# Kernel optimization log

Hardware: AMD Instinct MI355X
Metric: run time of the kernel (lower is better)

The kernel has to match this reference:

```python
import jax, jax.numpy as jnp
import numpy as np

Nq, Ns, D, H, S, B, MS, MB = 30000, 400, 128, 128, 200, 256, 4, 4
P = H + 3 * D  # pred_in_feature = 512


def _lin(k, out_f, in_f):
    sc = 1.0 / np.sqrt(in_f)
    return sc * jax.random.normal(k, (out_f, in_f), jnp.float32)


def setup_inputs() -> dict:
    key = jax.random.key(0)
    ks = jax.random.split(key, 40)
    inp = {}
    inp['q_emb'] = 0.1 * jax.random.normal(ks[0], (Nq, D), jnp.float32)
    inp['s_emb'] = 0.1 * jax.random.normal(ks[1], (Ns, D), jnp.float32)
    inp['ans_emb'] = jax.random.normal(ks[2], (4, D), jnp.float32)
    inp['label_emb'] = jax.random.normal(ks[3], (2, D), jnp.float32)
    inp['gru_Wi'] = _lin(ks[4], 3 * H, 5 * D)
    inp['gru_Wh'] = _lin(ks[5], 3 * H, H)
    inp['gru_bi'] = jnp.zeros((3 * H,), jnp.float32)
    inp['gru_bh'] = jnp.zeros((3 * H,), jnp.float32)
    for i, nm in enumerate(['s2s', 's2q', 'q2q', 'q2s']):
        inp[nm + '_W'] = _lin(ks[6 + i], D, D)
        inp[nm + '_b'] = jnp.zeros((D,), jnp.float32)
    inp['l1_W'] = _lin(ks[10], P, P); inp['l1_b'] = jnp.zeros((P,), jnp.float32)
    inp['l2_W'] = _lin(ks[11], P, P); inp['l2_b'] = jnp.zeros((P,), jnp.float32)
    inp['out_W'] = _lin(ks[12], 1, P); inp['out_b'] = jnp.zeros((1,), jnp.float32)
    inp['test_mask'] = jnp.ones((S, B), jnp.float32)
    inp['valid_mask'] = jnp.ones((S, B), jnp.float32)
    inp['local_test_mask'] = jnp.ones((S, B), jnp.float32)
    inp['subject_mask'] = jnp.ones((S, B, MB), jnp.float32)
    inp['q_mask'] = jnp.ones((Nq, MS), jnp.float32)
    inp['labels'] = jnp.round(jax.random.uniform(ks[13], (S, B), jnp.float32))
    inp['ans'] = jax.random.randint(ks[14], (S, B), 0, 4, jnp.int32)
    inp['correct_ans'] = jax.random.randint(ks[15], (S, B), 0, 4, jnp.int32)
    inp['subject_ids'] = jax.random.randint(ks[16], (S, B, MB), 0, Ns, jnp.int32)
    inp['q_ids'] = jax.random.randint(ks[17], (S, B), 0, Nq, jnp.int32)
    q_map = jax.random.randint(ks[18], (Nq, MS), 0, Ns, jnp.int32)
    inp['q_map'] = q_map
    inp['edge_q'] = jnp.repeat(jnp.arange(Nq, dtype=jnp.int32), MS)  # [Nq*MS]
    inp['edge_s'] = q_map.reshape(-1)  # subject segment id per edge
    return inp


def reference(q_emb, s_emb, ans_emb, label_emb, gru_Wi, gru_Wh, gru_bi, gru_bh,
              s2s_W, s2s_b, s2q_W, s2q_b, q2q_W, q2q_b, q2s_W, q2s_b,
              l1_W, l1_b, l2_W, l2_b, out_W, out_b,
              test_mask, valid_mask, local_test_mask, subject_mask, q_mask, labels,
              ans, correct_ans, subject_ids, q_ids, q_map, edge_q, edge_s):
    n_subject = s_emb.shape[0]
    # --- GCN layer 1: question -> subject aggregation (fused segment mean) ---
    q2s_proj = q_emb @ q2s_W.T + q2s_b                      # [Nq, D]
    sums = jax.ops.segment_sum(q2s_proj[edge_q], edge_s, num_segments=n_subject)
    cnts = jax.ops.segment_sum(jnp.ones_like(edge_s, q_emb.dtype), edge_s,
                               num_segments=n_subject)       # [Ns]
    nq_s = sums / jnp.maximum(cnts, 1.0)[:, None]            # mean over neighbor questions
    sq_s = s_emb @ s2s_W.T + s2s_b
    subjects_1 = jnp.where(cnts[:, None] > 0, jnp.tanh(nq_s + sq_s), 0.0)  # [Ns, D]
    # --- GCN layer 2: subject -> question aggregation ---
    nq = jnp.sum(subjects_1[q_map] * q_mask[..., None], axis=1) / \
         jnp.sum(q_mask, axis=-1, keepdims=True)             # [Nq, D]
    questions_1 = jnp.tanh(nq @ s2q_W.T + s2q_b + q_emb @ q2q_W.T + q2q_b)
    # --- sequence features ---
    mask = (test_mask * valid_mask * local_test_mask)[..., None]  # [S,B,1]
    subjects = jnp.sum(subjects_1[subject_ids] * subject_mask[..., None], axis=2)  # [S,B,D]
    questions = questions_1[q_ids]                            # [S,B,D]
    ans_embed = ans_emb[ans] * mask
    correct_ans_embed = ans_emb[correct_ans]
    label_embed = label_emb[labels.astype(jnp.int32)] * mask
    lstm_input = jnp.concatenate(
        [ans_embed, correct_ans_embed, label_embed, questions, subjects], axis=-1)  # [S,B,5D]
    # --- GRU (PyTorch gate layout: r|z|n), dropout=0 / eval mode ---
    xp = lstm_input @ gru_Wi.T + gru_bi                      # [S,B,3H]
    hdim = gru_Wh.shape[1]
    h0 = jnp.zeros((lstm_input.shape[1], hdim), lstm_input.dtype)

    def step(h, xp_t):
        gh = h @ gru_Wh.T + gru_bh
        xr, xz, xn = jnp.split(xp_t, 3, axis=-1)
        hr, hz, hn = jnp.split(gh, 3, axis=-1)
        r = jax.nn.sigmoid(xr + hr)
        z = jax.nn.sigmoid(xz + hz)
        n = jnp.tanh(xn + r * hn)
        h_new = (1.0 - z) * n + z * h
        return h_new, h_new

    _, outs = jax.lax.scan(step, h0, xp)                     # [S,B,H]
    forward_ht = jnp.concatenate([h0[None], outs[:-1]], axis=0)  # shifted hidden states
    # --- prediction head with residual ---
    pred_input = jnp.concatenate(
        [questions, subjects, forward_ht, correct_ans_embed], axis=-1)  # [S,B,P]
    h1 = jax.nn.relu(pred_input @ l1_W.T + l1_b)
    h2 = jax.nn.relu(h1 @ l2_W.T + l2_b)
    logits = ((h2 + pred_input) @ out_W.T + out_b)[..., 0]   # [S,B]
    # BCEWithLogits: softplus(x) - x*y
    per_elem = jax.nn.softplus(logits) - logits * labels
    mask2d = mask[..., 0]
    loss = jnp.mean(per_elem * mask2d) / jnp.mean(mask2d)
    probs = jax.nn.sigmoid(logits)
    return loss, probs
```

## Files before the change

kernel.cpp:

```cpp
#include <hip/hip_runtime.h>
#include <hip/hip_bf16.h>
#include <math.h>

#define NQ 30000
#define NS 400
#define DD 128
#define HH 128
#define SS 200
#define BB 256
#define MSq 4
#define MBs 4
#define PP 512
#define SB (SS*BB)
#define G3 384
#define QPB 16
#define REPL 8
#define TST (48*2048)

typedef __hip_bfloat16 bf16;
typedef __attribute__((ext_vector_type(8))) short bf16x8;
typedef __attribute__((ext_vector_type(4))) float f32x4;
typedef __attribute__((ext_vector_type(4))) _Float16 f16x4;

__device__ __forceinline__ float sigf(float x){ return 1.0f/(1.0f+expf(-x)); }
__device__ __forceinline__ float sigf2(float x){ return 1.0f/(1.0f+__expf(-x)); }
__device__ __forceinline__ float tanhf2(float x){ return 1.0f - 2.0f/(__expf(2.0f*x)+1.0f); }

__global__ __launch_bounds__(128) void tables_k(const float* __restrict__ ans_emb,
        const float* __restrict__ label_emb, const float* __restrict__ Wi,
        float* __restrict__ Tans, float* __restrict__ Tcae, float* __restrict__ Tlab){
  int j = blockIdx.x*128 + threadIdx.x;
  if (j >= G3) return;
  const float* wr = Wi + (size_t)j*640;
  for (int a=0;a<4;a++){
    float acc=0.f;
    for (int k=0;k<DD;k++) acc += ans_emb[a*DD+k]*wr[k];
    Tans[a*G3+j]=acc;
  }
  for (int a=0;a<4;a++){
    float acc=0.f;
    for (int k=0;k<DD;k++) acc += ans_emb[a*DD+k]*wr[128+k];
    Tcae[a*G3+j]=acc;
  }
  for (int l=0;l<2;l++){
    float acc=0.f;
    for (int k=0;k<DD;k++) acc += label_emb[l*DD+k]*wr[256+k];
    Tlab[l*G3+j]=acc;
  }
}

__global__ __launch_bounds__(256) void conv_w_k(const float* __restrict__ l1W,
        const float* __restrict__ l2W, const float* __restrict__ Wi,
        bf16* __restrict__ l1Wb, bf16* __restrict__ l2Wb, bf16* __restrict__ WiB){
  int i = blockIdx.x*256 + threadIdx.x;
  if (i < 512*512){
    l1Wb[i] = __float2bfloat16(l1W[i]);
    l2Wb[i] = __float2bfloat16(l2W[i]);
  }
  if (i < 384*256){
    int j = i >> 8, k = i & 255;
    WiB[i] = __float2bfloat16(Wi[j*640 + 384 + k]);
  }
}

__global__ __launch_bounds__(128) void q2s_scatter(const float* __restrict__ q_emb,
        const float* __restrict__ W, const float* __restrict__ bias,
        const int* __restrict__ q_map, float* __restrict__ sums, float* __restrict__ cnts){
  __shared__ float qe[QPB][DD];
  int q0 = blockIdx.x*QPB;
  int tid = threadIdx.x;
  float* S = sums + (size_t)(blockIdx.x & (REPL-1))*51200;
  float* C = cnts + (size_t)(blockIdx.x & (REPL-1))*400;
  for (int r=0;r<QPB;r++) qe[r][tid] = q_emb[(size_t)(q0+r)*DD + tid];
  __syncthreads();
  float acc[QPB];
  #pragma unroll
  for (int r=0;r<QPB;r++) acc[r] = bias[tid];
  const float4* wr = (const float4*)(W + (size_t)tid*DD);
  #pragma unroll 4
  for (int k4=0;k4<DD/4;k4++){
    float4 w = wr[k4];
    #pragma unroll
    for (int r=0;r<QPB;r++){
      acc[r] += w.x*qe[r][k4*4] + w.y*qe[r][k4*4+1] + w.z*qe[r][k4*4+2] + w.w*qe[r][k4*4+3];
    }
  }
  for (int r=0;r<QPB;r++){
    int q = q0+r;
    #pragma unroll
    for (int m=0;m<MSq;m++){
      int s = q_map[q*MSq+m];
      atomicAdd(&S[(size_t)s*DD + tid], acc[r]);
      if (tid==0) atomicAdd(&C[s], 1.0f);
    }
  }
}

__global__ __launch_bounds__(128) void subjects1_k(const float* __restrict__ s_emb,
        const float* __restrict__ W, const float* __restrict__ bias,
        const float* __restrict__ sums, const float* __restrict__ cnts,
        float* __restrict__ out){
  __shared__ float se[DD];
  int s = blockIdx.x; int tid = threadIdx.x;
  se[tid] = s_emb[(size_t)s*DD+tid];
  __syncthreads();
  float acc = bias[tid];
  const float4* wr = (const float4*)(W + (size_t)tid*DD);
  for (int k4=0;k4<DD/4;k4++){
    float4 w = wr[k4];
    acc += w.x*se[k4*4] + w.y*se[k4*4+1] + w.z*se[k4*4+2] + w.w*se[k4*4+3];
  }
  float c = 0.f, sm = 0.f;
  #pragma unroll
  for (int r=0;r<REPL;r++){
    c  += cnts[r*400 + s];
    sm += sums[(size_t)r*51200 + (size_t)s*DD + tid];
  }
  float v = 0.f;
  if (c > 0.f) v = tanhf(sm/fmaxf(c,1.f) + acc);
  out[(size_t)s*DD+tid] = v;
}

__global__ __launch_bounds__(128) void questions1_k(const float* __restrict__ q_emb,
        const float* __restrict__ subj1, const int* __restrict__ q_map,
        const float* __restrict__ q_mask,
        const float* __restrict__ s2qW, const float* __restrict__ s2qb,
        const float* __restrict__ q2qW, const float* __restrict__ q2qb,
        bf16* __restrict__ q1out){
  __shared__ float qe[QPB][DD];
  __shared__ float nq[QPB][DD];
  int q0 = blockIdx.x*QPB; int tid = threadIdx.x;
  for (int r=0;r<QPB;r++){
    int q = q0+r;
    qe[r][tid] = q_emb[(size_t)q*DD+tid];
    float sum=0.f, wsum=0.f;
    #pragma unroll
    for (int m=0;m<MSq;m++){
      float w = q_mask[q*MSq+m];
      sum += subj1[(size_t)q_map[q*MSq+m]*DD + tid]*w;
      wsum += w;
    }
    nq[r][tid] = sum / wsum;
  }
  __syncthreads();
  float acc[QPB];
  #pragma unroll
  for (int r=0;r<QPB;r++) acc[r] = s2qb[tid]+q2qb[tid];
  const float4* w1 = (const float4*)(s2qW + (size_t)tid*DD);
  const float4* w2 = (const float4*)(q2qW + (size_t)tid*DD);
  #pragma unroll 2
  for (int k4=0;k4<DD/4;k4++){
    float4 a = w1[k4]; float4 b = w2[k4];
    #pragma unroll
    for (int r=0;r<QPB;r++){
      acc[r] += a.x*nq[r][k4*4] + a.y*nq[r][k4*4+1] + a.z*nq[r][k4*4+2] + a.w*nq[r][k4*4+3]
              + b.x*qe[r][k4*4] + b.y*qe[r][k4*4+1] + b.z*qe[r][k4*4+2] + b.w*qe[r][k4*4+3];
    }
  }
  for (int r=0;r<QPB;r++) q1out[(size_t)(q0+r)*DD+tid] = __float2bfloat16(tanhf(acc[r]));
}

__global__ __launch_bounds__(128) void assemble_k(const bf16* __restrict__ q1,
        const float* __restrict__ subj1, const float* __restrict__ ans_emb,
        const int* __restrict__ cans, const int* __restrict__ sub_ids,
        const float* __restrict__ sub_mask, const int* __restrict__ q_ids,
        bf16* __restrict__ pred){
  int i = blockIdx.x; int d = threadIdx.x;
  size_t base = (size_t)i*PP;
  pred[base + d] = q1[(size_t)q_ids[i]*DD + d];
  float s = 0.f;
  #pragma unroll
  for (int m=0;m<MBs;m++)
    s += subj1[(size_t)sub_ids[i*MBs+m]*DD+d]*sub_mask[i*MBs+m];
  pred[base+128+d] = __float2bfloat16(s);
  pred[base+384+d] = __float2bfloat16(ans_emb[(size_t)cans[i]*DD + d]);
}

#define MFMA_CORE(A_, lda_, B_, ldb_, K_) \
  int lane = threadIdx.x & 63; int wid = threadIdx.x >> 6; \
  int wy = wid >> 1, wx = wid & 1; \
  int mbase = blockIdx.x*128 + wy*64; \
  int nbase = blockIdx.y*128 + wx*64; \
  int lr = lane & 15, kg = (lane >> 4) * 8; \
  f32x4 acc[4][4]; \
  _Pragma("unroll") for (int i=0;i<4;i++) _Pragma("unroll") for (int j=0;j<4;j++) acc[i][j] = (f32x4){0.f,0.f,0.f,0.f}; \
  for (int k=0; k<(K_); k+=32){ \
    bf16x8 af[4], bfr[4]; \
    _Pragma("unroll") for (int mi=0;mi<4;mi++) \
      af[mi] = *(const bf16x8*)((A_) + (size_t)(mbase+mi*16+lr)*(lda_) + k + kg); \
    _Pragma("unroll") for (int ni=0;ni<4;ni++) \
      bfr[ni] = *(const bf16x8*)((B_) + (size_t)(nbase+ni*16+lr)*(ldb_) + k + kg); \
    _Pragma("unroll") for (int mi=0;mi<4;mi++) \
      _Pragma("unroll") for (int ni=0;ni<4;ni++) \
        acc[mi][ni] = __builtin_amdgcn_mfma_f32_16x16x32_bf16(af[mi], bfr[ni], acc[mi][ni], 0, 0, 0); \
  }

__global__ __launch_bounds__(256) void gemm_xp(const bf16* __restrict__ pred,
        const bf16* __restrict__ WiB, const float* __restrict__ bi,
        const float* __restrict__ bh,
        const float* __restrict__ Tans, const float* __restrict__ Tcae,
        const float* __restrict__ Tlab,
        const float* __restrict__ tm, const float* __restrict__ vm,
        const float* __restrict__ lm,
        const int* __restrict__ ans, const int* __restrict__ cans,
        const float* __restrict__ labels, _Float16* __restrict__ xp2){
  MFMA_CORE(pred, PP, WiB, 256, 256)
  #pragma unroll
  for (int mi=0;mi<4;mi++){
    #pragma unroll
    for (int r=0;r<4;r++){
      int row = mbase + mi*16 + (lane>>4)*4 + r;
      int t = row >> 8, b = row & 255;
      size_t rowpart = ((size_t)t*48 + (b>>4)*3)*2048 + (b&15);
      float mk = tm[row]*vm[row]*lm[row];
      int a = ans[row], ca = cans[row], lb = (int)labels[row];
      #pragma unroll
      for (int ni=0;ni<4;ni++){
        int c = nbase + ni*16 + lr;
        int g = c >> 7, dd = c & 127;
        float v = acc[mi][ni][r] + bi[c]
            + mk*Tans[a*G3+c] + Tcae[ca*G3+c] + mk*Tlab[lb*G3+c];
        if (g < 2) v += bh[c];
        xp2[rowpart + (size_t)(g*2048 + dd*16)] = (_Float16)v;
      }
    }
  }
}

__global__ __launch_bounds__(256) void gemm_l1(const bf16* __restrict__ pred,
        const bf16* __restrict__ Wb, const float* __restrict__ bias,
        bf16* __restrict__ h1){
  MFMA_CORE(pred, PP, Wb, PP, PP)
  #pragma unroll
  for (int mi=0;mi<4;mi++){
    #pragma unroll
    for (int ni=0;ni<4;ni++){
      int c = nbase + ni*16 + lr;
      float bia = bias[c];
      #pragma unroll
      for (int r=0;r<4;r++){
        int row = mbase + mi*16 + (lane>>4)*4 + r;
        h1[(size_t)row*PP + c] = __float2bfloat16(fmaxf(acc[mi][ni][r] + bia, 0.f));
      }
    }
  }
}

__global__ __launch_bounds__(256) void gemm_l2_logits(const bf16* __restrict__ h1,
        const bf16* __restrict__ Wb, const float* __restrict__ bias,
        const bf16* __restrict__ pred, const float* __restrict__ outW,
        float* __restrict__ logits){
  MFMA_CORE(h1, PP, Wb, PP, PP)
  #pragma unroll
  for (int mi=0;mi<4;mi++){
    #pragma unroll
    for (int r=0;r<4;r++){
      int row = mbase + mi*16 + (lane>>4)*4 + r;
      float p = 0.f;
      #pragma unroll
      for (int ni=0;ni<4;ni++){
        int c = nbase + ni*16 + lr;
        float h2v = fmaxf(acc[mi][ni][r] + bias[c], 0.f);
        p += (h2v + __bfloat162float(pred[(size_t)row*PP + c])) * outW[c];
      }
      p += __shfl_xor(p,1);
      p += __shfl_xor(p,2);
      p += __shfl_xor(p,4);
      p += __shfl_xor(p,8);
      if (lr == 0) atomicAdd(&logits[row], p);
    }
  }
}

__global__ __launch_bounds__(512, 1) void gru_scan_mfma(const _Float16* __restrict__ xp2,
        const float* __restrict__ Wh, const float* __restrict__ bh,
        bf16* __restrict__ pred){
  __shared__ __align__(16) char hbf[8192];
  const int tid  = threadIdx.x;
  const int lane = tid & 63;
  const int w    = tid >> 6;
  const int lr   = lane & 15;
  const int lg   = lane >> 4;
  const int d    = w*16 + lr;
  const int bg0  = blockIdx.x * 16;

  union U8 { bf16x8 v; unsigned short s[8]; };
  bf16x8 wf0[4], wf1[4], wf2[4];
  #pragma unroll
  for (int kk=0; kk<4; kk++){
    #pragma unroll
    for (int g=0; g<3; g++){
      const float* src = Wh + (size_t)(g*HH + d)*HH + kk*32 + lg*8;
      U8 u;
      #pragma unroll
      for (int j=0;j<8;j++){
        bf16 bv = __float2bfloat16(src[j]);
        u.s[j] = reinterpret_cast<unsigned short&>(bv);
      }
      if (g==0) wf0[kk]=u.v; else if (g==1) wf1[kk]=u.v; else wf2[kk]=u.v;
    }
  }
  const float bh2 = bh[2*HH+d];

  int rdaddr[4];
  #pragma unroll
  for (int kk=0;kk<4;kk++) rdaddr[kk] = lr*256 + ((kk*64 + lg*16) ^ ((lr&7)<<4));
  int wraddr[4];
  #pragma unroll
  for (int q=0;q<4;q++){
    int B_ = lg*4 + q;
    wraddr[q] = B_*256 + ((2*d) ^ ((B_&7)<<4));
  }
  const int fB = tid >> 4, fblk = tid & 15;
  const int faddr = fB*256 + ((fblk*16) ^ ((fB&7)<<4));
  bf16* fptr = pred + ((size_t)bg0 + fB)*PP + 256 + fblk*8;
  const size_t PSTRIDE = (size_t)BB*PP;

  float h0=0.f, h1v=0.f, h2v=0.f, h3v=0.f;
  ((unsigned long long*)hbf)[tid]       = 0ULL;
  ((unsigned long long*)hbf)[tid + 512] = 0ULL;

  const _Float16* x0 = xp2 + (size_t)blockIdx.x*3*2048 + d*16 + lg*4;
  f16x4 xrA = *(const f16x4*)(x0);
  f16x4 xzA = *(const f16x4*)(x0 + 2048);
  f16x4 xnA = *(const f16x4*)(x0 + 4096);
  f16x4 xrB = *(const f16x4*)(x0 + TST);
  f16x4 xzB = *(const f16x4*)(x0 + TST + 2048);
  f16x4 xnB = *(const f16x4*)(x0 + TST + 4096);
  const _Float16* xtr = x0 + 2*(size_t)TST;
  const _Float16* xtz = xtr + 2048;
  const _Float16* xtn = xtr + 4096;

  __syncthreads();

#define GATEQ(Q, CR, CZ, CN, HV) { \
    float r  = sigf2((float)(CR) + ac0[Q]); \
    float zg = sigf2((float)(CZ) + ac1[Q]); \
    float n  = tanhf2((float)(CN) + r*(ac2[Q] + bh2)); \
    HV = (1.f - zg)*n + zg*HV; }

#define GSTEP(RO_, WO_, XR, XZ, XN) { \
    f32x4 ac0 = (f32x4){0.f,0.f,0.f,0.f}, ac1 = ac0, ac2 = ac0; \
    _Pragma("unroll") for (int kk=0; kk<4; kk++){ \
      bf16x8 a = *(const bf16x8*)(hbf + (RO_) + rdaddr[kk]); \
      ac0 = __builtin_amdgcn_mfma_f32_16x16x32_bf16(a, wf0[kk], ac0, 0,0,0); \
      ac1 = __builtin_amdgcn_mfma_f32_16x16x32_bf16(a, wf1[kk], ac1, 0,0,0); \
      ac2 = __builtin_amdgcn_mfma_f32_16x16x32_bf16(a, wf2[kk], ac2, 0,0,0); \
    } \
    if (tid < 256){   \
      int4 hv = *(const int4*)(hbf + (RO_) + faddr); \
      *(int4*)fptr = hv; \
    } \
    fptr += PSTRIDE; \
    GATEQ(0, (XR).x, (XZ).x, (XN).x, h0) \
    GATEQ(1, (XR).y, (XZ).y, (XN).y, h1v) \
    GATEQ(2, (XR).z, (XZ).z, (XN).z, h2v) \
    GATEQ(3, (XR).w, (XZ).w, (XN).w, h3v) \
    *(bf16*)(hbf + (WO_) + wraddr[0]) = __float2bfloat16(h0); \
    *(bf16*)(hbf + (WO_) + wraddr[1]) = __float2bfloat16(h1v); \
    *(bf16*)(hbf + (WO_) + wraddr[2]) = __float2bfloat16(h2v); \
    *(bf16*)(hbf + (WO_) + wraddr[3]) = __float2bfloat16(h3v); \
    XR = *(const f16x4*)(xtr); XZ = *(const f16x4*)(xtz); XN = *(const f16x4*)(xtn); \
    xtr += TST; xtz += TST; xtn += TST; \
    asm volatile("s_waitcnt lgkmcnt(0)" ::: "memory"); \
    __builtin_amdgcn_s_barrier(); \
    __builtin_amdgcn_sched_barrier(0); \
  }

  for (int t=0; t<SS; t+=2){
    GSTEP(0,    4096, xrA, xzA, xnA)
    GSTEP(4096, 0,    xrB, xzB, xnB)
  }
#undef GSTEP
#undef GATEQ
}

__global__ __launch_bounds__(256) void loss_probs_k(const float* __restrict__ logits,
        const float* __restrict__ labels, const float* __restrict__ tm,
        const float* __restrict__ vm, const float* __restrict__ lm,
        const float* __restrict__ out_b, float* __restrict__ out,
        float* __restrict__ lacc){
  int i = blockIdx.x*256 + threadIdx.x;
  float x = logits[i] + out_b[0];
  float lb = labels[i];
  float mk = tm[i]*vm[i]*lm[i];
  float sp = fmaxf(x,0.f) + log1pf(expf(-fabsf(x)));
  float pe = (sp - x*lb)*mk;
  out[1+i] = sigf(x);
  float v0 = pe, v1 = mk;
  for (int o=32;o>0;o>>=1){ v0 += __shfl_down(v0,o); v1 += __shfl_down(v1,o); }
  if ((threadIdx.x & 63)==0){ atomicAdd(&lacc[0], v0); atomicAdd(&lacc[1], v1); }
}

__global__ void finalize_k(const float* __restrict__ lacc, float* __restrict__ out){
  out[0] = lacc[0]/lacc[1];
}

extern "C" void kernel_launch(void* const* d_in, const int* in_sizes, int n_in,
                              void* d_out, int out_size, void* d_ws, size_t ws_size,
                              hipStream_t stream) {
  const float* q_emb   = (const float*)d_in[0];
  const float* s_emb   = (const float*)d_in[1];
  const float* ans_emb = (const float*)d_in[2];
  const float* lab_emb = (const float*)d_in[3];
  const float* gru_Wi  = (const float*)d_in[4];
  const float* gru_Wh  = (const float*)d_in[5];
  const float* gru_bi  = (const float*)d_in[6];
  const float* gru_bh  = (const float*)d_in[7];
  const float* s2s_W   = (const float*)d_in[8];
  const float* s2s_b   = (const float*)d_in[9];
  const float* s2q_W   = (const float*)d_in[10];
  const float* s2q_b   = (const float*)d_in[11];
  const float* q2q_W   = (const float*)d_in[12];
  const float* q2q_b   = (const float*)d_in[13];
  const float* q2s_W   = (const float*)d_in[14];
  const float* q2s_b   = (const float*)d_in[15];
  const float* l1_W    = (const float*)d_in[16];
  const float* l1_b    = (const float*)d_in[17];
  const float* l2_W    = (const float*)d_in[18];
  const float* l2_b    = (const float*)d_in[19];
  const float* out_W   = (const float*)d_in[20];
  const float* out_b   = (const float*)d_in[21];
  const float* tm      = (const float*)d_in[22];
  const float* vm      = (const float*)d_in[23];
  const float* lm      = (const float*)d_in[24];
  const float* smask   = (const float*)d_in[25];
  const float* q_mask  = (const float*)d_in[26];
  const float* labels  = (const float*)d_in[27];
  const int*   ans     = (const int*)d_in[28];
  const int*   cans    = (const int*)d_in[29];
  const int*   sub_ids = (const int*)d_in[30];
  const int*   q_ids   = (const int*)d_in[31];
  const int*   q_map   = (const int*)d_in[32];

  char* wsb = (char*)d_ws;
  size_t off = 0;
  auto alloc = [&](size_t bytes) -> char* {
    char* p = wsb + off;
    off += (bytes + 255) & ~(size_t)255;
    return p;
  };
  float* sums   = (float*)alloc((size_t)REPL*51200*4);
  float* cnts   = (float*)alloc((size_t)REPL*400*4);
  float* subj1  = (float*)alloc(51200*4);
  float* Tans   = (float*)alloc(4*G3*4);
  float* Tcae   = (float*)alloc(4*G3*4);
  float* Tlab   = (float*)alloc(2*G3*4);
  float* lacc   = (float*)alloc(2*4);
  float* logits = (float*)alloc((size_t)SB*4);
  bf16*  l1Wb   = (bf16*) alloc((size_t)512*512*2);
  bf16*  l2Wb   = (bf16*) alloc((size_t)512*512*2);
  bf16*  WiB    = (bf16*) alloc((size_t)384*256*2);
  bf16*  q1     = (bf16*) alloc((size_t)NQ*DD*2);
  bf16*  pred   = (bf16*) alloc((size_t)SB*PP*2);
  size_t xp2_bytes = ((size_t)SS+2)*TST*2;
  size_t h1_bytes  = (size_t)SB*PP*2;
  char*  xh     = alloc(xp2_bytes > h1_bytes ? xp2_bytes : h1_bytes);
  _Float16* xp2 = (_Float16*)xh;
  bf16*  h1     = (bf16*)xh;
  float* out    = (float*)d_out;

  hipMemsetAsync(sums, 0, (size_t)REPL*(51200+400)*sizeof(float), stream);
  hipMemsetAsync(lacc, 0, 2*sizeof(float), stream);
  hipMemsetAsync(logits, 0, (size_t)SB*sizeof(float), stream);

  tables_k<<<dim3(3), dim3(128), 0, stream>>>(ans_emb, lab_emb, gru_Wi, Tans, Tcae, Tlab);
  conv_w_k<<<dim3(1024), dim3(256), 0, stream>>>(l1_W, l2_W, gru_Wi, l1Wb, l2Wb, WiB);
  q2s_scatter<<<dim3(NQ/QPB), dim3(128), 0, stream>>>(q_emb, q2s_W, q2s_b, q_map, sums, cnts);
  subjects1_k<<<dim3(NS), dim3(128), 0, stream>>>(s_emb, s2s_W, s2s_b, sums, cnts, subj1);
  questions1_k<<<dim3(NQ/QPB), dim3(128), 0, stream>>>(q_emb, subj1, q_map, q_mask,
                                                       s2q_W, s2q_b, q2q_W, q2q_b, q1);
  assemble_k<<<dim3(SB), dim3(128), 0, stream>>>(q1, subj1, ans_emb, cans, sub_ids, smask, q_ids, pred);
  gemm_xp<<<dim3(400,3), dim3(256), 0, stream>>>(pred, WiB, gru_bi, gru_bh, Tans, Tcae, Tlab,
                                                 tm, vm, lm, ans, cans, labels, xp2);
  gru_scan_mfma<<<dim3(16), dim3(512), 0, stream>>>(xp2, gru_Wh, gru_bh, pred);
  gemm_l1<<<dim3(400,4), dim3(256), 0, stream>>>(pred, l1Wb, l1_b, h1);
  gemm_l2_logits<<<dim3(400,4), dim3(256), 0, stream>>>(h1, l2Wb, l2_b, pred, out_W, logits);
  loss_probs_k<<<dim3(SB/256), dim3(256), 0, stream>>>(logits, labels, tm, vm, lm, out_b, out, lacc);
  finalize_k<<<dim3(1), dim3(1), 0, stream>>>(lacc, out);
}
```

Before: 933.7 us.

## Split GRU scan over 32 blocks, fuse l1/l2 GEMMs via LDS, deepen xp prefetch

The GRU scan now runs on 32 blocks of 8 batch columns each instead of 16 blocks of 16, with the xp buffer relaid out to match. Each step keeps eight time steps of input gates prefetched in registers. The two head GEMMs are fused into one kernel: h1 stays in swizzled LDS, the residual dot with out_W is computed from the A fragments during layer 1, and the h1 round trip through global memory is removed. gemm_xp loops over the three gate tiles inside one block, so only 400 blocks launch. Only half the MFMA rows are used in the scan, so compute efficiency per block drops in exchange for more blocks running in parallel. The fused head runs at one 512-thread block per CU with 64 KB of LDS.

```diff
diff --git a/kernel.cpp b/kernel.cpp
--- a/kernel.cpp
+++ b/kernel.cpp
@@ -15,7 +15,8 @@
 #define G3 384
 #define QPB 16
 #define REPL 8
-#define TST (48*2048)
+#define GBLK 32
+#define TST3 (GBLK*3*1024)
 
 typedef __hip_bfloat16 bf16;
 typedef __attribute__((ext_vector_type(8))) short bf16x8;
@@ -25,6 +26,10 @@
 __device__ __forceinline__ float sigf(float x){ return 1.0f/(1.0f+expf(-x)); }
 __device__ __forceinline__ float sigf2(float x){ return 1.0f/(1.0f+__expf(-x)); }
 __device__ __forceinline__ float tanhf2(float x){ return 1.0f - 2.0f/(__expf(2.0f*x)+1.0f); }
+__device__ __forceinline__ float bfu2f(unsigned short u){
+  unsigned int x = ((unsigned int)u)<<16;
+  return __uint_as_float(x);
+}
 
 __global__ __launch_bounds__(128) void tables_k(const float* __restrict__ ans_emb,
         const float* __restrict__ label_emb, const float* __restrict__ Wi,
@@ -176,25 +181,6 @@
   pred[base+384+d] = __float2bfloat16(ans_emb[(size_t)cans[i]*DD + d]);
 }
 
-#define MFMA_CORE(A_, lda_, B_, ldb_, K_) \
-  int lane = threadIdx.x & 63; int wid = threadIdx.x >> 6; \
-  int wy = wid >> 1, wx = wid & 1; \
-  int mbase = blockIdx.x*128 + wy*64; \
-  int nbase = blockIdx.y*128 + wx*64; \
-  int lr = lane & 15, kg = (lane >> 4) * 8; \
-  f32x4 acc[4][4]; \
-  _Pragma("unroll") for (int i=0;i<4;i++) _Pragma("unroll") for (int j=0;j<4;j++) acc[i][j] = (f32x4){0.f,0.f,0.f,0.f}; \
-  for (int k=0; k<(K_); k+=32){ \
-    bf16x8 af[4], bfr[4]; \
-    _Pragma("unroll") for (int mi=0;mi<4;mi++) \
-      af[mi] = *(const bf16x8*)((A_) + (size_t)(mbase+mi*16+lr)*(lda_) + k + kg); \
-    _Pragma("unroll") for (int ni=0;ni<4;ni++) \
-      bfr[ni] = *(const bf16x8*)((B_) + (size_t)(nbase+ni*16+lr)*(ldb_) + k + kg); \
-    _Pragma("unroll") for (int mi=0;mi<4;mi++) \
-      _Pragma("unroll") for (int ni=0;ni<4;ni++) \
-        acc[mi][ni] = __builtin_amdgcn_mfma_f32_16x16x32_bf16(af[mi], bfr[ni], acc[mi][ni], 0, 0, 0); \
-  }
-
 __global__ __launch_bounds__(256) void gemm_xp(const bf16* __restrict__ pred,
         const bf16* __restrict__ WiB, const float* __restrict__ bi,
         const float* __restrict__ bh,
@@ -203,76 +189,167 @@
         const float* __restrict__ tm, const float* __restrict__ vm,
         const float* __restrict__ lm,
         const int* __restrict__ ans, const int* __restrict__ cans,
-        const float* __restrict__ labels, _Float16* __restrict__ xp2){
-  MFMA_CORE(pred, PP, WiB, 256, 256)
-  #pragma unroll
-  for (int mi=0;mi<4;mi++){
-    #pragma unroll
-    for (int r=0;r<4;r++){
-      int row = mbase + mi*16 + (lane>>4)*4 + r;
-      int t = row >> 8, b = row & 255;
-      size_t rowpart = ((size_t)t*48 + (b>>4)*3)*2048 + (b&15);
-      float mk = tm[row]*vm[row]*lm[row];
-      int a = ans[row], ca = cans[row], lb = (int)labels[row];
+        const float* __restrict__ labels, _Float16* __restrict__ xp3){
+  int lane = threadIdx.x & 63; int wid = threadIdx.x >> 6;
+  int wy = wid >> 1, wx = wid & 1;
+  int mbase = blockIdx.x*128 + wy*64;
+  int lr = lane & 15, kg = (lane >> 4) * 8;
+  for (int ny=0; ny<3; ny++){
+    int nbase = ny*128 + wx*64;
+    f32x4 acc[4][4];
+    #pragma unroll
+    for (int i=0;i<4;i++)
+      #pragma unroll
+      for (int j=0;j<4;j++) acc[i][j] = (f32x4){0.f,0.f,0.f,0.f};
+    for (int k=0; k<256; k+=32){
+      bf16x8 af[4], bfr[4];
+      #pragma unroll
+      for (int mi=0;mi<4;mi++)
+        af[mi] = *(const bf16x8*)(pred + (size_t)(mbase+mi*16+lr)*PP + k + kg);
+      #pragma unroll
+      for (int ni=0;ni<4;ni++)
+        bfr[ni] = *(const bf16x8*)(WiB + (size_t)(nbase+ni*16+lr)*256 + k + kg);
+      #pragma unroll
+      for (int mi=0;mi<4;mi++)
+        #pragma unroll
+        for (int ni=0;ni<4;ni++)
+          acc[mi][ni] = __builtin_amdgcn_mfma_f32_16x16x32_bf16(af[mi], bfr[ni], acc[mi][ni], 0, 0, 0);
+    }
+    #pragma unroll
+    for (int mi=0;mi<4;mi++){
+      #pragma unroll
+      for (int r=0;r<4;r++){
+        int row = mbase + mi*16 + (lane>>4)*4 + r;
+        int t = row >> 8, b = row & 255;
+        size_t base = (((size_t)t*GBLK + (b>>3))*3)*1024 + (b&7);
+        float mk = tm[row]*vm[row]*lm[row];
+        int a = ans[row], ca = cans[row], lb = (int)labels[row];
+        #pragma unroll
+        for (int ni=0;ni<4;ni++){
+          int c = nbase + ni*16 + lr;
+          int g = c >> 7, dd = c & 127;
+          float v = acc[mi][ni][r] + bi[c]
+              + mk*Tans[a*G3+c] + Tcae[ca*G3+c] + mk*Tlab[lb*G3+c];
+          if (g < 2) v += bh[c];
+          xp3[base + (size_t)(g*1024 + dd*8)] = (_Float16)v;
+        }
+      }
+    }
+  }
+}
+
+__global__ __launch_bounds__(512, 1) void gemm_l1l2(const bf16* __restrict__ pred,
+        const bf16* __restrict__ W1, const float* __restrict__ b1,
+        const bf16* __restrict__ W2, const float* __restrict__ b2,
+        const float* __restrict__ outW, float* __restrict__ logits){
+  __shared__ __align__(16) char hl[64*1024];
+  const int lane = threadIdx.x & 63;
+  const int wx = threadIdx.x >> 6;
+  const int nbase = wx*64;
+  const int mbase = blockIdx.x*64;
+  const int lr = lane & 15, lg = lane >> 4, kg = lg*8;
+
+  {
+    f32x4 acc[4][4];
+    #pragma unroll
+    for (int i=0;i<4;i++)
+      #pragma unroll
+      for (int j=0;j<4;j++) acc[i][j] = (f32x4){0.f,0.f,0.f,0.f};
+    float pres[4] = {0.f,0.f,0.f,0.f};
+    for (int k=0; k<512; k+=32){
+      bf16x8 af[4], bfr[4];
+      #pragma unroll
+      for (int mi=0;mi<4;mi++)
+        af[mi] = *(const bf16x8*)(pred + (size_t)(mbase+mi*16+lr)*PP + k + kg);
+      #pragma unroll
+      for (int ni=0;ni<4;ni++)
+        bfr[ni] = *(const bf16x8*)(W1 + (size_t)(nbase+ni*16+lr)*PP + k + kg);
+      #pragma unroll
+      for (int mi=0;mi<4;mi++)
+        #pragma unroll
+        for (int ni=0;ni<4;ni++)
+          acc[mi][ni] = __builtin_amdgcn_mfma_f32_16x16x32_bf16(af[mi], bfr[ni], acc[mi][ni], 0, 0, 0);
+      if (wx == 0){
+        float4 o0 = *(const float4*)(outW + k + kg);
+        float4 o1 = *(const float4*)(outW + k + kg + 4);
+        #pragma unroll
+        for (int mi=0;mi<4;mi++){
+          const unsigned short* au = (const unsigned short*)&af[mi];
+          pres[mi] += bfu2f(au[0])*o0.x + bfu2f(au[1])*o0.y + bfu2f(au[2])*o0.z + bfu2f(au[3])*o0.w
+                    + bfu2f(au[4])*o1.x + bfu2f(au[5])*o1.y + bfu2f(au[6])*o1.z + bfu2f(au[7])*o1.w;
+        }
+      }
+    }
+    #pragma unroll
+    for (int mi=0;mi<4;mi++){
       #pragma unroll
       for (int ni=0;ni<4;ni++){
         int c = nbase + ni*16 + lr;
-        int g = c >> 7, dd = c & 127;
-        float v = acc[mi][ni][r] + bi[c]
-            + mk*Tans[a*G3+c] + Tcae[ca*G3+c] + mk*Tlab[lb*G3+c];
-        if (g < 2) v += bh[c];
-        xp2[rowpart + (size_t)(g*2048 + dd*16)] = (_Float16)v;
-      }
-    }
-  }
-}
-
-__global__ __launch_bounds__(256) void gemm_l1(const bf16* __restrict__ pred,
-        const bf16* __restrict__ Wb, const float* __restrict__ bias,
-        bf16* __restrict__ h1){
-  MFMA_CORE(pred, PP, Wb, PP, PP)
-  #pragma unroll
-  for (int mi=0;mi<4;mi++){
-    #pragma unroll
-    for (int ni=0;ni<4;ni++){
-      int c = nbase + ni*16 + lr;
-      float bia = bias[c];
+        float bia = b1[c];
+        #pragma unroll
+        for (int r=0;r<4;r++){
+          int rw = mi*16 + lg*4 + r;
+          int addr = (rw*1024 + c*2) ^ ((rw&7)<<4);
+          *(bf16*)(hl + addr) = __float2bfloat16(fmaxf(acc[mi][ni][r] + bia, 0.f));
+        }
+      }
+    }
+    if (wx == 0){
+      #pragma unroll
+      for (int mi=0;mi<4;mi++){
+        float v = pres[mi];
+        v += __shfl_xor(v, 16);
+        v += __shfl_xor(v, 32);
+        if (lg == 0) atomicAdd(&logits[mbase + mi*16 + lr], v);
+      }
+    }
+  }
+  __syncthreads();
+  {
+    f32x4 acc[4][4];
+    #pragma unroll
+    for (int i=0;i<4;i++)
+      #pragma unroll
+      for (int j=0;j<4;j++) acc[i][j] = (f32x4){0.f,0.f,0.f,0.f};
+    for (int k=0; k<512; k+=32){
+      bf16x8 af[4], bfr[4];
+      #pragma unroll
+      for (int mi=0;mi<4;mi++){
+        int rw = mi*16 + lr;
+        int addr = (rw*1024 + (k+kg)*2) ^ ((rw&7)<<4);
+        af[mi] = *(const bf16x8*)(hl + addr);
+      }
+      #pragma unroll
+      for (int ni=0;ni<4;ni++)
+        bfr[ni] = *(const bf16x8*)(W2 + (size_t)(nbase+ni*16+lr)*PP + k + kg);
+      #pragma unroll
+      for (int mi=0;mi<4;mi++)
+        #pragma unroll
+        for (int ni=0;ni<4;ni++)
+          acc[mi][ni] = __builtin_amdgcn_mfma_f32_16x16x32_bf16(af[mi], bfr[ni], acc[mi][ni], 0, 0, 0);
+    }
+    #pragma unroll
+    for (int mi=0;mi<4;mi++){
       #pragma unroll
       for (int r=0;r<4;r++){
-        int row = mbase + mi*16 + (lane>>4)*4 + r;
-        h1[(size_t)row*PP + c] = __float2bfloat16(fmaxf(acc[mi][ni][r] + bia, 0.f));
-      }
-    }
-  }
-}
-
-__global__ __launch_bounds__(256) void gemm_l2_logits(const bf16* __restrict__ h1,
-        const bf16* __restrict__ Wb, const float* __restrict__ bias,
-        const bf16* __restrict__ pred, const float* __restrict__ outW,
-        float* __restrict__ logits){
-  MFMA_CORE(h1, PP, Wb, PP, PP)
-  #pragma unroll
-  for (int mi=0;mi<4;mi++){
-    #pragma unroll
-    for (int r=0;r<4;r++){
-      int row = mbase + mi*16 + (lane>>4)*4 + r;
-      float p = 0.f;
-      #pragma unroll
-      for (int ni=0;ni<4;ni++){
-        int c = nbase + ni*16 + lr;
-        float h2v = fmaxf(acc[mi][ni][r] + bias[c], 0.f);
-        p += (h2v + __bfloat162float(pred[(size_t)row*PP + c])) * outW[c];
-      }
-      p += __shfl_xor(p,1);
-      p += __shfl_xor(p,2);
-      p += __shfl_xor(p,4);
-      p += __shfl_xor(p,8);
-      if (lr == 0) atomicAdd(&logits[row], p);
-    }
-  }
-}
-
-__global__ __launch_bounds__(512, 1) void gru_scan_mfma(const _Float16* __restrict__ xp2,
+        int row = mbase + mi*16 + lg*4 + r;
+        float p = 0.f;
+        #pragma unroll
+        for (int ni=0;ni<4;ni++){
+          int c = nbase + ni*16 + lr;
+          p += fmaxf(acc[mi][ni][r] + b2[c], 0.f) * outW[c];
+        }
+        p += __shfl_xor(p,1);
+        p += __shfl_xor(p,2);
+        p += __shfl_xor(p,4);
+        p += __shfl_xor(p,8);
+        if (lr == 0) atomicAdd(&logits[row], p);
+      }
+    }
+  }
+}
+
+__global__ __launch_bounds__(512, 1) void gru_scan_mfma(const _Float16* __restrict__ xp3,
         const float* __restrict__ Wh, const float* __restrict__ bh,
         bf16* __restrict__ pred){
   __shared__ __align__(16) char hbf[8192];
@@ -282,7 +359,7 @@
   const int lr   = lane & 15;
   const int lg   = lane >> 4;
   const int d    = w*16 + lr;
-  const int bg0  = blockIdx.x * 16;
+  const int bg0  = blockIdx.x * 8;
 
   union U8 { bf16x8 v; unsigned short s[8]; };
   bf16x8 wf0[4], wf1[4], wf2[4];
@@ -320,16 +397,14 @@
   ((unsigned long long*)hbf)[tid]       = 0ULL;
   ((unsigned long long*)hbf)[tid + 512] = 0ULL;
 
-  const _Float16* x0 = xp2 + (size_t)blockIdx.x*3*2048 + d*16 + lg*4;
-  f16x4 xrA = *(const f16x4*)(x0);
-  f16x4 xzA = *(const f16x4*)(x0 + 2048);
-  f16x4 xnA = *(const f16x4*)(x0 + 4096);
-  f16x4 xrB = *(const f16x4*)(x0 + TST);
-  f16x4 xzB = *(const f16x4*)(x0 + TST + 2048);
-  f16x4 xnB = *(const f16x4*)(x0 + TST + 4096);
-  const _Float16* xtr = x0 + 2*(size_t)TST;
-  const _Float16* xtz = xtr + 2048;
-  const _Float16* xtn = xtr + 4096;
+  const char* xb = (const char*)(xp3 + (size_t)blockIdx.x*3*1024 + d*8 + (lg&1)*4);
+
+#define GSET(s) \
+  f16x4 x##s##r = *(const f16x4*)(xb + (size_t)(s)*TST3*2); \
+  f16x4 x##s##z = *(const f16x4*)(xb + (size_t)(s)*TST3*2 + 2048); \
+  f16x4 x##s##n = *(const f16x4*)(xb + (size_t)(s)*TST3*2 + 4096);
+  GSET(0) GSET(1) GSET(2) GSET(3) GSET(4) GSET(5) GSET(6) GSET(7)
+#undef GSET
 
   __syncthreads();
 
@@ -339,7 +414,7 @@
     float n  = tanhf2((float)(CN) + r*(ac2[Q] + bh2)); \
     HV = (1.f - zg)*n + zg*HV; }
 
-#define GSTEP(RO_, WO_, XR, XZ, XN) { \
+#define GSTEP(s, RO_, WO_) { \
     f32x4 ac0 = (f32x4){0.f,0.f,0.f,0.f}, ac1 = ac0, ac2 = ac0; \
     _Pragma("unroll") for (int kk=0; kk<4; kk++){ \
       bf16x8 a = *(const bf16x8*)(hbf + (RO_) + rdaddr[kk]); \
@@ -347,29 +422,39 @@
       ac1 = __builtin_amdgcn_mfma_f32_16x16x32_bf16(a, wf1[kk], ac1, 0,0,0); \
       ac2 = __builtin_amdgcn_mfma_f32_16x16x32_bf16(a, wf2[kk], ac2, 0,0,0); \
     } \
-    if (tid < 256){   \
+    if (tid < 128){   \
       int4 hv = *(const int4*)(hbf + (RO_) + faddr); \
       *(int4*)fptr = hv; \
     } \
     fptr += PSTRIDE; \
-    GATEQ(0, (XR).x, (XZ).x, (XN).x, h0) \
-    GATEQ(1, (XR).y, (XZ).y, (XN).y, h1v) \
-    GATEQ(2, (XR).z, (XZ).z, (XN).z, h2v) \
-    GATEQ(3, (XR).w, (XZ).w, (XN).w, h3v) \
-    *(bf16*)(hbf + (WO_) + wraddr[0]) = __float2bfloat16(h0); \
-    *(bf16*)(hbf + (WO_) + wraddr[1]) = __float2bfloat16(h1v); \
-    *(bf16*)(hbf + (WO_) + wraddr[2]) = __float2bfloat16(h2v); \
-    *(bf16*)(hbf + (WO_) + wraddr[3]) = __float2bfloat16(h3v); \
-    XR = *(const f16x4*)(xtr); XZ = *(const f16x4*)(xtz); XN = *(const f16x4*)(xtn); \
-    xtr += TST; xtz += TST; xtn += TST; \
+    GATEQ(0, x##s##r.x, x##s##z.x, x##s##n.x, h0) \
+    GATEQ(1, x##s##r.y, x##s##z.y, x##s##n.y, h1v) \
+    GATEQ(2, x##s##r.z, x##s##z.z, x##s##n.z, h2v) \
+    GATEQ(3, x##s##r.w, x##s##z.w, x##s##n.w, h3v) \
+    if (lg < 2){ \
+      *(bf16*)(hbf + (WO_) + wraddr[0]) = __float2bfloat16(h0); \
+      *(bf16*)(hbf + (WO_) + wraddr[1]) = __float2bfloat16(h1v); \
+      *(bf16*)(hbf + (WO_) + wraddr[2]) = __float2bfloat16(h2v); \
+      *(bf16*)(hbf + (WO_) + wraddr[3]) = __float2bfloat16(h3v); \
+    } \
+    x##s##r = *(const f16x4*)(xb + (size_t)((s)+8)*TST3*2); \
+    x##s##z = *(const f16x4*)(xb + (size_t)((s)+8)*TST3*2 + 2048); \
+    x##s##n = *(const f16x4*)(xb + (size_t)((s)+8)*TST3*2 + 4096); \
     asm volatile("s_waitcnt lgkmcnt(0)" ::: "memory"); \
     __builtin_amdgcn_s_barrier(); \
     __builtin_amdgcn_sched_barrier(0); \
   }
 
-  for (int t=0; t<SS; t+=2){
-    GSTEP(0,    4096, xrA, xzA, xnA)
-    GSTEP(4096, 0,    xrB, xzB, xnB)
+  for (int it=0; it<SS/8; ++it){
+    GSTEP(0, 0,    4096)
+    GSTEP(1, 4096, 0)
+    GSTEP(2, 0,    4096)
+    GSTEP(3, 4096, 0)
+    GSTEP(4, 0,    4096)
+    GSTEP(5, 4096, 0)
+    GSTEP(6, 0,    4096)
+    GSTEP(7, 4096, 0)
+    xb += (size_t)8*TST3*2;
   }
 #undef GSTEP
 #undef GATEQ
@@ -453,11 +538,7 @@
   bf16*  WiB    = (bf16*) alloc((size_t)384*256*2);
   bf16*  q1     = (bf16*) alloc((size_t)NQ*DD*2);
   bf16*  pred   = (bf16*) alloc((size_t)SB*PP*2);
-  size_t xp2_bytes = ((size_t)SS+2)*TST*2;
-  size_t h1_bytes  = (size_t)SB*PP*2;
-  char*  xh     = alloc(xp2_bytes > h1_bytes ? xp2_bytes : h1_bytes);
-  _Float16* xp2 = (_Float16*)xh;
-  bf16*  h1     = (bf16*)xh;
+  _Float16* xp3 = (_Float16*)alloc(((size_t)SS+8)*TST3*2);
   float* out    = (float*)d_out;
 
   hipMemsetAsync(sums, 0, (size_t)REPL*(51200+400)*sizeof(float), stream);
@@ -471,11 +552,10 @@
   questions1_k<<<dim3(NQ/QPB), dim3(128), 0, stream>>>(q_emb, subj1, q_map, q_mask,
                                                        s2q_W, s2q_b, q2q_W, q2q_b, q1);
   assemble_k<<<dim3(SB), dim3(128), 0, stream>>>(q1, subj1, ans_emb, cans, sub_ids, smask, q_ids, pred);
-  gemm_xp<<<dim3(400,3), dim3(256), 0, stream>>>(pred, WiB, gru_bi, gru_bh, Tans, Tcae, Tlab,
-                                                 tm, vm, lm, ans, cans, labels, xp2);
-  gru_scan_mfma<<<dim3(16), dim3(512), 0, stream>>>(xp2, gru_Wh, gru_bh, pred);
-  gemm_l1<<<dim3(400,4), dim3(256), 0, stream>>>(pred, l1Wb, l1_b, h1);
-  gemm_l2_logits<<<dim3(400,4), dim3(256), 0, stream>>>(h1, l2Wb, l2_b, pred, out_W, logits);
+  gemm_xp<<<dim3(400), dim3(256), 0, stream>>>(pred, WiB, gru_bi, gru_bh, Tans, Tcae, Tlab,
+                                               tm, vm, lm, ans, cans, labels, xp3);
+  gru_scan_mfma<<<dim3(GBLK), dim3(512), 0, stream>>>(xp3, gru_Wh, gru_bh, pred);
+  gemm_l1l2<<<dim3(SB/64), dim3(512), 0, stream>>>(pred, l1Wb, l1_b, l2Wb, l2_b, out_W, logits);
   loss_probs_k<<<dim3(SB/256), dim3(256), 0, stream>>>(logits, labels, tm, vm, lm, out_b, out, lacc);
   finalize_k<<<dim3(1), dim3(1), 0, stream>>>(lacc, out);
 }
```

Measured after the change: 922.8 us. About the same (-1.2%).
